# Kernel tuning notes

Measured on AMD Instinct MI355X. Metric: run time of the kernel, lower is better.

## Reference

```python
import jax, jax.numpy as jnp
import numpy as np

B, T, D, H, BAND = 2, 4096, 512, 8, 16
LN_EPS = 1e-5


def setup_inputs() -> dict:
    key = jax.random.key(0)
    k0, k1, k2 = jax.random.split(key, 3)
    x = jax.random.normal(k0, (B, T, D), jnp.float32)
    # nn.MultiheadAttention params: packed in_proj [3D, D] and out_proj [D, D]
    w_in = jax.random.normal(k1, (3 * D, D), jnp.float32) * 0.02
    b_in = jnp.zeros((3 * D,), jnp.float32)
    w_out = jax.random.normal(k2, (D, D), jnp.float32) * 0.02
    b_out = jnp.zeros((D,), jnp.float32)
    ln_g = jnp.ones((D,), jnp.float32)
    ln_b = jnp.zeros((D,), jnp.float32)
    return dict(x=x, ln_g=ln_g, ln_b=ln_b, w_in=w_in, b_in=b_in,
                w_out=w_out, b_out=b_out)


def reference(x, ln_g, ln_b, w_in, b_in, w_out, b_out):
    Bq, Tq, Dq = x.shape
    dh = Dq // H
    # LayerNorm
    mu = jnp.mean(x, axis=-1, keepdims=True)
    var = jnp.mean(jnp.square(x - mu), axis=-1, keepdims=True)
    h = (x - mu) * jax.lax.rsqrt(var + LN_EPS) * ln_g + ln_b
    # packed QKV projection (torch Linear: y = h @ W^T + b)
    qkv = h @ w_in.T + b_in                      # [B, T, 3D]
    q, k, v = jnp.split(qkv, 3, axis=-1)
    to_heads = lambda a: a.reshape(Bq, Tq, H, dh).transpose(0, 2, 1, 3)  # [B,H,T,dh]
    q, k, v = to_heads(q), to_heads(k), to_heads(v)
    # band-gather: each query t attends to keys in [t-BAND, t+BAND]
    Wn = 2 * BAND + 1
    offs = jnp.arange(-BAND, BAND + 1)
    idx = jnp.arange(Tq)[:, None] + offs[None, :]          # [T, Wn]
    valid = (idx >= 0) & (idx < Tq)                        # [T, Wn]
    idx_c = jnp.clip(idx, 0, Tq - 1)
    k_win = k[:, :, idx_c]                                 # [B,H,T,Wn,dh]
    v_win = v[:, :, idx_c]                                 # [B,H,T,Wn,dh]
    scale = 1.0 / np.sqrt(dh).astype(np.float32)
    scores = jnp.einsum('bhtd,bhtwd->bhtw', q * scale, k_win)
    scores = jnp.where(valid[None, None], scores, -jnp.inf)
    p = jax.nn.softmax(scores, axis=-1)                    # [B,H,T,Wn]
    o = jnp.einsum('bhtw,bhtwd->bhtd', p, v_win)           # [B,H,T,dh]
    o = o.transpose(0, 2, 1, 3).reshape(Bq, Tq, Dq)
    y = o @ w_out.T + b_out
    return x + y
```

## Files before the change

kernel.cpp:

```cpp
#include <hip/hip_runtime.h>
#include <hip/hip_bf16.h>

#define T_ 4096
#define D_ 512
#define H_ 8
#define BAND 16
#define G1_K 512

typedef float f32x4 __attribute__((ext_vector_type(4)));
typedef __bf16 bf16x8 __attribute__((ext_vector_type(8)));
typedef unsigned short us8 __attribute__((ext_vector_type(8)));
typedef unsigned short us4 __attribute__((ext_vector_type(4)));

__device__ __forceinline__ unsigned short f2b(float f) {
  union { float f; unsigned u; } v; v.f = f;
  unsigned r = v.u + 0x7fffu + ((v.u >> 16) & 1u);
  return (unsigned short)(r >> 16);
}

__device__ __forceinline__ f32x4 mfma16(bf16x8 a, bf16x8 b, f32x4 c) {
  return __builtin_amdgcn_mfma_f32_16x16x32_bf16(a, b, c, 0, 0, 0);
}

#define GLD16(gp, lp) __builtin_amdgcn_global_load_lds( \
    (const __attribute__((address_space(1))) void*)(gp), \
    (__attribute__((address_space(3))) void*)(lp), 16, 0, 0)

__global__ __launch_bounds__(256) void prep_k(const float* __restrict__ x,
                                              const float* __restrict__ g,
                                              const float* __restrict__ bt,
                                              const float* __restrict__ win,
                                              const float* __restrict__ wout,
                                              unsigned short* __restrict__ h,
                                              unsigned short* __restrict__ winb,
                                              unsigned short* __restrict__ woutb) {
  int bx = blockIdx.x;
  if (bx >= 2048) {
    int i = (bx - 2048) * 256 + threadIdx.x;
    const int n1 = 3 * D_ * D_ / 4;
    if (i < n1) {
      float4 v = ((const float4*)win)[i];
      us4 o; o.x = f2b(v.x); o.y = f2b(v.y); o.z = f2b(v.z); o.w = f2b(v.w);
      ((us4*)winb)[i] = o;
    } else {
      int j = i - n1;
      float4 v = ((const float4*)wout)[j];
      us4 o; o.x = f2b(v.x); o.y = f2b(v.y); o.z = f2b(v.z); o.w = f2b(v.w);
      ((us4*)woutb)[j] = o;
    }
    return;
  }
  int wave = threadIdx.x >> 6, lane = threadIdx.x & 63;
  size_t row = (size_t)bx * 4 + wave;
  const float4* xr = (const float4*)(x + row * D_);
  float4 a = xr[lane * 2], b = xr[lane * 2 + 1];
  float s = a.x + a.y + a.z + a.w + b.x + b.y + b.z + b.w;
  #pragma unroll
  for (int o = 32; o; o >>= 1) s += __shfl_xor(s, o, 64);
  float mu = s * (1.0f / D_);
  float d0 = a.x - mu, d1 = a.y - mu, d2 = a.z - mu, d3 = a.w - mu;
  float d4 = b.x - mu, d5 = b.y - mu, d6 = b.z - mu, d7 = b.w - mu;
  float q = d0*d0 + d1*d1 + d2*d2 + d3*d3 + d4*d4 + d5*d5 + d6*d6 + d7*d7;
  #pragma unroll
  for (int o = 32; o; o >>= 1) q += __shfl_xor(q, o, 64);
  float rstd = rsqrtf(q * (1.0f / D_) + 1e-5f);
  const float4* gr = (const float4*)g;
  const float4* br = (const float4*)bt;
  float4 g0 = gr[lane * 2], g1 = gr[lane * 2 + 1];
  float4 b0 = br[lane * 2], b1 = br[lane * 2 + 1];
  us8 o8;
  o8[0] = f2b(d0 * rstd * g0.x + b0.x);
  o8[1] = f2b(d1 * rstd * g0.y + b0.y);
  o8[2] = f2b(d2 * rstd * g0.z + b0.z);
  o8[3] = f2b(d3 * rstd * g0.w + b0.w);
  o8[4] = f2b(d4 * rstd * g1.x + b1.x);
  o8[5] = f2b(d5 * rstd * g1.y + b1.y);
  o8[6] = f2b(d6 * rstd * g1.z + b1.z);
  o8[7] = f2b(d7 * rstd * g1.w + b1.w);
  *((us8*)(h + row * D_) + lane) = o8;
}

#define OPA 0
#define OPB 1

__device__ __forceinline__ void stg(const unsigned short* __restrict__ gb,
                                    unsigned short* lds, int slot, int op, int h, int tt,
                                    int rl0, int u0, int su) {
  #pragma unroll
  for (int j = 0; j < 2; ++j) {
    const unsigned short* g = gb + (size_t)(h * 128 + rl0 + 64 * j) * G1_K + tt * 64 + su;
    unsigned short* lp = lds + slot * 32768 + op * 16384 + h * 8192 + (rl0 + 64 * j) * 64 + u0 * 8;
    GLD16(g, lp);
  }
}

#define VMC4 asm volatile("s_waitcnt vmcnt(4)" ::: "memory")
#define VMC0 asm volatile("s_waitcnt vmcnt(0)" ::: "memory")

#define PHASE(SLOT, PH, STAGE_STMT, WAIT_STMT) do {                                        \
    if ((PH) == 0) {                                                                       \
      _Pragma("unroll") for (int nf = 0; nf < 4; ++nf) {                                   \
        breg[nf][0] = *(const bf16x8*)(lds + (SLOT)*32768 + boff + nf*1024 + swz0);        \
        breg[nf][1] = *(const bf16x8*)(lds + (SLOT)*32768 + boff + nf*1024 + swz1);        \
      }                                                                                    \
    }                                                                                      \
    bf16x8 a0k0 = *(const bf16x8*)(lds + (SLOT)*32768 + aoff + (2*(PH))*1024 + swz0);      \
    bf16x8 a0k1 = *(const bf16x8*)(lds + (SLOT)*32768 + aoff + (2*(PH))*1024 + swz1);      \
    bf16x8 a1k0 = *(const bf16x8*)(lds + (SLOT)*32768 + aoff + (2*(PH)+1)*1024 + swz0);    \
    bf16x8 a1k1 = *(const bf16x8*)(lds + (SLOT)*32768 + aoff + (2*(PH)+1)*1024 + swz1);    \
    STAGE_STMT;                                                                            \
    __builtin_amdgcn_s_barrier();                                                          \
    asm volatile("s_waitcnt lgkmcnt(0)" ::: "memory");                                     \
    __builtin_amdgcn_sched_barrier(0);                                                     \
    __builtin_amdgcn_s_setprio(1);                                                         \
    _Pragma("unroll") for (int nf = 0; nf < 4; ++nf) {                                     \
      acc[2*(PH)][nf]   = mfma16(a0k0, breg[nf][0], acc[2*(PH)][nf]);                      \
      acc[2*(PH)][nf]   = mfma16(a0k1, breg[nf][1], acc[2*(PH)][nf]);                      \
      acc[2*(PH)+1][nf] = mfma16(a1k0, breg[nf][0], acc[2*(PH)+1][nf]);                    \
      acc[2*(PH)+1][nf] = mfma16(a1k1, breg[nf][1], acc[2*(PH)+1][nf]);                    \
    }                                                                                      \
    __builtin_amdgcn_s_setprio(0);                                                         \
    __builtin_amdgcn_sched_barrier(0);                                                     \
    WAIT_STMT;                                                                             \
    __builtin_amdgcn_s_barrier();                                                          \
  } while (0)

__global__ __launch_bounds__(512, 2) void gemm_qkv8(const unsigned short* __restrict__ A,
                                                    const unsigned short* __restrict__ Bw,
                                                    const float* __restrict__ bias,
                                                    unsigned short* __restrict__ C) {
  extern __shared__ char smem[];
  unsigned short* lds = (unsigned short*)smem;
  int tid = threadIdx.x;
  int lane = tid & 63, wave = tid >> 6;
  int wm = wave >> 2, wn = wave & 3;
  int fr = lane & 15, fq = lane >> 4;
  int d = blockIdx.x;
  int l = (d & 7) * 24 + (d >> 3);
  int bm = l / 6, bn = l % 6;

  const unsigned short* Ag = A + (size_t)bm * 256 * G1_K;
  const unsigned short* Bg = Bw + (size_t)bn * 256 * G1_K;

  int rl0 = tid >> 3, u0 = tid & 7;
  int su = (u0 ^ (rl0 & 7)) * 8;

  int aoff = wm * 8192 + fr * 64;
  int boff = 16384 + (wn >> 1) * 8192 + ((wn & 1) * 64 + fr) * 64;
  int swz0 = (fq ^ (fr & 7)) * 8;
  int swz1 = ((4 + fq) ^ (fr & 7)) * 8;

  f32x4 acc[8][4] = {};
  bf16x8 breg[4][2];

  stg(Bg, lds, 0, OPB, 0, 0, rl0, u0, su);
  stg(Bg, lds, 0, OPB, 1, 0, rl0, u0, su);
  stg(Ag, lds, 0, OPA, 0, 0, rl0, u0, su);
  stg(Ag, lds, 0, OPA, 1, 0, rl0, u0, su);
  stg(Bg, lds, 1, OPB, 0, 1, rl0, u0, su);
  stg(Bg, lds, 1, OPB, 1, 1, rl0, u0, su);
  VMC4;
  __builtin_amdgcn_s_barrier();

  #pragma unroll 1
  for (int i = 0; i < 3; ++i) {
    int t = 2 * i;
    PHASE(0, 0, stg(Ag, lds, 1, OPA, 0, t + 1, rl0, u0, su), (void)0);
    PHASE(0, 1, stg(Ag, lds, 1, OPA, 1, t + 1, rl0, u0, su), (void)0);
    PHASE(0, 2, stg(Bg, lds, 0, OPB, 0, t + 2, rl0, u0, su), (void)0);
    PHASE(0, 3, stg(Bg, lds, 0, OPB, 1, t + 2, rl0, u0, su), VMC4);
    PHASE(1, 0, stg(Ag, lds, 0, OPA, 0, t + 2, rl0, u0, su), (void)0);
    PHASE(1, 1, stg(Ag, lds, 0, OPA, 1, t + 2, rl0, u0, su), (void)0);
    PHASE(1, 2, stg(Bg, lds, 1, OPB, 0, t + 3, rl0, u0, su), (void)0);
    PHASE(1, 3, stg(Bg, lds, 1, OPB, 1, t + 3, rl0, u0, su), VMC4);
  }
  PHASE(0, 0, stg(Ag, lds, 1, OPA, 0, 7, rl0, u0, su), (void)0);
  PHASE(0, 1, stg(Ag, lds, 1, OPA, 1, 7, rl0, u0, su), (void)0);
  PHASE(0, 2, (void)0, (void)0);
  PHASE(0, 3, (void)0, VMC0);
  PHASE(1, 0, (void)0, (void)0);
  PHASE(1, 1, (void)0, (void)0);
  PHASE(1, 2, (void)0, (void)0);
  PHASE(1, 3, (void)0, (void)0);

  int rbase = bm * 256 + wm * 128 + fq * 4;
  int cbase = bn * 256 + wn * 64 + fr;
  float bv[4];
  #pragma unroll
  for (int nf = 0; nf < 4; ++nf) bv[nf] = bias[cbase + nf * 16];
  #pragma unroll
  for (int mf = 0; mf < 8; ++mf)
    #pragma unroll
    for (int nf = 0; nf < 4; ++nf)
      #pragma unroll
      for (int r = 0; r < 4; ++r)
        C[(size_t)(rbase + mf * 16 + r) * 1536 + cbase + nf * 16] = f2b(acc[mf][nf][r] + bv[nf]);
}

__global__ __launch_bounds__(512, 2) void attn_out_k(const unsigned short* __restrict__ qkv,
                                                     const unsigned short* __restrict__ woutb,
                                                     const float* __restrict__ bout,
                                                     const float* __restrict__ x,
                                                     float* __restrict__ out) {
  extern __shared__ char smem2[];
  unsigned short* lds = (unsigned short*)smem2;
  int tid = threadIdx.x;
  int lane = tid & 63, wave = tid >> 6;
  int fr = lane & 15, fq = lane >> 4;
  int r0g = blockIdx.x * 32;
  int bb = r0g >> 12;
  int t0 = r0g & (T_ - 1);
  size_t rowbase = (size_t)bb * T_;

  unsigned short* Ob = lds + 41984;

  #pragma unroll 1
  for (int rd = 0; rd < 2; ++rd) {
    #pragma unroll
    for (int i = 0; i < 8; ++i) {
      int idx = i * 512 + tid;
      int s   = idx >> 10;
      int rem = idx & 1023;
      int ten = rem >> 9;
      int c   = rem & 511;
      int r   = c >> 3, u = c & 7;
      int hh  = 4 * rd + s;
      int tg  = t0 - BAND + r;
      us8 v8 = {0, 0, 0, 0, 0, 0, 0, 0};
      if (tg >= 0 && tg < T_)
        v8 = *(const us8*)(qkv + (rowbase + tg) * 1536 + (ten ? 1024 : 512) + hh * 64 + u * 8);
      if (ten == 0) {
        *(us8*)(lds + s * 8192 + r * 64 + ((u ^ (r & 7)) << 3)) = v8;
      } else {
        int base = s * 8192 + 4096;
        #pragma unroll
        for (int j = 0; j < 8; ++j)
          lds[base + (u * 8 + j) * 64 + (((r >> 3) ^ u) << 3) + (r & 7)] = v8[j];
      }
    }
    __syncthreads();

    {
      int s  = wave >> 1;
      int hh = 4 * rd + s;
      int qg = wave & 1;
      int q  = t0 + qg * 16 + fr;

      const unsigned short* qp = qkv + (rowbase + q) * 1536 + hh * 64;
      bf16x8 qf0 = *(const bf16x8*)(qp + fq * 8);
      bf16x8 qf1 = *(const bf16x8*)(qp + 32 + fq * 8);

      const unsigned short* Kb = lds + s * 8192;
      f32x4 sacc[4];
      #pragma unroll
      for (int mf = 0; mf < 4; ++mf) sacc[mf] = (f32x4){0.f, 0.f, 0.f, 0.f};
      #pragma unroll
      for (int mf = 0; mf < 4; ++mf) {
        bf16x8 k0 = *(const bf16x8*)(Kb + (mf * 16 + fr) * 64 + ((fq ^ (fr & 7)) << 3));
        bf16x8 k1 = *(const bf16x8*)(Kb + (mf * 16 + fr) * 64 + (((4 + fq) ^ (fr & 7)) << 3));
        sacc[mf] = mfma16(k0, qf0, sacc[mf]);
        sacc[mf] = mfma16(k1, qf1, sacc[mf]);
      }

      float ev[4][4];
      float vmx = -1e30f;
      #pragma unroll
      for (int mf = 0; mf < 4; ++mf)
        #pragma unroll
        for (int r = 0; r < 4; ++r) {
          int tk = t0 - BAND + mf * 16 + fq * 4 + r;
          bool ok = (tk >= q - BAND) && (tk <= q + BAND) && (tk >= 0) && (tk < T_);
          float v = ok ? sacc[mf][r] * 0.125f : -1e30f;
          ev[mf][r] = v;
          vmx = fmaxf(vmx, v);
        }
      vmx = fmaxf(vmx, __shfl_xor(vmx, 16, 64));
      vmx = fmaxf(vmx, __shfl_xor(vmx, 32, 64));
      float ssum = 0.f;
      #pragma unroll
      for (int mf = 0; mf < 4; ++mf)
        #pragma unroll
        for (int r = 0; r < 4; ++r) {
          float e = (ev[mf][r] > -1e29f) ? exp2f((ev[mf][r] - vmx) * 1.44269504f) : 0.f;
          ev[mf][r] = e;
          ssum += e;
        }
      ssum += __shfl_xor(ssum, 16, 64);
      ssum += __shfl_xor(ssum, 32, 64);
      float inv = 1.0f / ssum;

      unsigned short* Pb = lds + 32768 + wave * 1152;
      #pragma unroll
      for (int mf = 0; mf < 4; ++mf)
        #pragma unroll
        for (int r = 0; r < 4; ++r)
          Pb[fr * 72 + mf * 16 + fq * 4 + r] = f2b(ev[mf][r] * inv);
      asm volatile("s_waitcnt lgkmcnt(0)" ::: "memory");
      __builtin_amdgcn_sched_barrier(0);

      const unsigned short* Vb = lds + s * 8192 + 4096;
      f32x4 oacc[4];
      #pragma unroll
      for (int cf = 0; cf < 4; ++cf) oacc[cf] = (f32x4){0.f, 0.f, 0.f, 0.f};
      #pragma unroll
      for (int kk = 0; kk < 2; ++kk) {
        bf16x8 pa = *(const bf16x8*)(Pb + fr * 72 + (kk * 4 + fq) * 8);
        #pragma unroll
        for (int cf = 0; cf < 4; ++cf) {
          int du = cf * 2 + (fr >> 3);
          bf16x8 vf = *(const bf16x8*)(Vb + (cf * 16 + fr) * 64 + (((kk * 4 + fq) ^ du) << 3));
          oacc[cf] = mfma16(pa, vf, oacc[cf]);
        }
      }

      #pragma unroll
      for (int cf = 0; cf < 4; ++cf)
        #pragma unroll
        for (int r = 0; r < 4; ++r) {
          int qq = qg * 16 + fq * 4 + r;
          int unit = hh * 8 + (((cf * 2 + (fr >> 3)) ^ (qq & 7)));
          Ob[qq * 512 + unit * 8 + (fr & 7)] = f2b(oacc[cf][r]);
        }
    }
    __syncthreads();
  }

  f32x4 acc[2][4];
  #pragma unroll
  for (int mf = 0; mf < 2; ++mf)
    #pragma unroll
    for (int nf = 0; nf < 4; ++nf) acc[mf][nf] = (f32x4){0.f, 0.f, 0.f, 0.f};

  const unsigned short* Bb = woutb + (size_t)(wave * 64) * 512;
  #pragma unroll 4
  for (int ks = 0; ks < 16; ++ks) {
    bf16x8 a0 = *(const bf16x8*)(Ob + (0 * 16 + fr) * 512 + (((ks * 4 + fq) ^ (fr & 7)) << 3));
    bf16x8 a1 = *(const bf16x8*)(Ob + (1 * 16 + fr) * 512 + (((ks * 4 + fq) ^ (fr & 7)) << 3));
    bf16x8 bfr[4];
    #pragma unroll
    for (int nf = 0; nf < 4; ++nf)
      bfr[nf] = *(const bf16x8*)(Bb + (size_t)(nf * 16 + fr) * 512 + ks * 32 + fq * 8);
    #pragma unroll
    for (int nf = 0; nf < 4; ++nf) {
      acc[0][nf] = mfma16(a0, bfr[nf], acc[0][nf]);
      acc[1][nf] = mfma16(a1, bfr[nf], acc[1][nf]);
    }
  }

  #pragma unroll
  for (int mf = 0; mf < 2; ++mf)
    #pragma unroll
    for (int nf = 0; nf < 4; ++nf) {
      int col = wave * 64 + nf * 16 + fr;
      float bv = bout[col];
      #pragma unroll
      for (int r = 0; r < 4; ++r) {
        size_t e = (size_t)(r0g + mf * 16 + fq * 4 + r) * 512 + col;
        out[e] = x[e] + acc[mf][nf][r] + bv;
      }
    }
}

extern "C" void kernel_launch(void* const* d_in, const int* in_sizes, int n_in,
                              void* d_out, int out_size, void* d_ws, size_t ws_size,
                              hipStream_t stream) {
  (void)in_sizes; (void)n_in; (void)out_size; (void)ws_size;
  const float* x     = (const float*)d_in[0];
  const float* ln_g  = (const float*)d_in[1];
  const float* ln_b  = (const float*)d_in[2];
  const float* w_in  = (const float*)d_in[3];
  const float* b_in  = (const float*)d_in[4];
  const float* w_out = (const float*)d_in[5];
  const float* b_out = (const float*)d_in[6];
  float* out = (float*)d_out;

  char* ws = (char*)d_ws;
  unsigned short* hb    = (unsigned short*)(ws);
  unsigned short* winb  = (unsigned short*)(ws + 8388608);
  unsigned short* woutb = (unsigned short*)(ws + 9961472);
  unsigned short* qkvb  = (unsigned short*)(ws + 10485760);

  (void)hipFuncSetAttribute((const void*)gemm_qkv8,
                            hipFuncAttributeMaxDynamicSharedMemorySize, 131072);
  (void)hipFuncSetAttribute((const void*)attn_out_k,
                            hipFuncAttributeMaxDynamicSharedMemorySize, 116736);

  prep_k<<<3072, 256, 0, stream>>>(x, ln_g, ln_b, w_in, w_out, hb, winb, woutb);
  gemm_qkv8<<<192, 512, 131072, stream>>>(hb, winb, b_in, qkvb);
  attn_out_k<<<256, 512, 116736, stream>>>(qkvb, woutb, b_out, x, out);
}
```

Baseline: 61.77 us.

## Shrink attention blocks to 16 rows, pass P via shuffles, remap block order

The attention+out-projection kernel now processes 16 query rows per block with 256 threads (one wave per head) instead of 32 rows with 512 threads. The key window drops to 48 rows (3 MFMA tiles), so less K/V is staged into LDS. The probability matrix moves from the LDS round-trip to lane shuffles. Block indices are permuted across the grid, and the LDS footprint drops so more blocks fit per CU. The trade-off is that each block redoes the halo K/V loads for fewer queries and re-reads the full W_out for only 16 rows, doubling W_out traffic.

```diff
diff --git a/kernel.cpp b/kernel.cpp
--- a/kernel.cpp
+++ b/kernel.cpp
@@ -197,7 +197,7 @@
         C[(size_t)(rbase + mf * 16 + r) * 1536 + cbase + nf * 16] = f2b(acc[mf][nf][r] + bv[nf]);
 }
 
-__global__ __launch_bounds__(512, 2) void attn_out_k(const unsigned short* __restrict__ qkv,
+__global__ __launch_bounds__(256, 2) void attn_out_k(const unsigned short* __restrict__ qkv,
                                                      const unsigned short* __restrict__ woutb,
                                                      const float* __restrict__ bout,
                                                      const float* __restrict__ x,
@@ -207,32 +207,40 @@
   int tid = threadIdx.x;
   int lane = tid & 63, wave = tid >> 6;
   int fr = lane & 15, fq = lane >> 4;
-  int r0g = blockIdx.x * 32;
+  int dd = blockIdx.x;
+  int lblk = (dd & 7) * 64 + (dd >> 3);
+  int r0g = lblk * 16;
   int bb = r0g >> 12;
   int t0 = r0g & (T_ - 1);
   size_t rowbase = (size_t)bb * T_;
 
-  unsigned short* Ob = lds + 41984;
+  unsigned short* Ob = lds + 28672;
 
   #pragma unroll 1
   for (int rd = 0; rd < 2; ++rd) {
+    if (rd) __syncthreads();
     #pragma unroll
-    for (int i = 0; i < 8; ++i) {
-      int idx = i * 512 + tid;
-      int s   = idx >> 10;
-      int rem = idx & 1023;
-      int ten = rem >> 9;
-      int c   = rem & 511;
-      int r   = c >> 3, u = c & 7;
-      int hh  = 4 * rd + s;
-      int tg  = t0 - BAND + r;
-      us8 v8 = {0, 0, 0, 0, 0, 0, 0, 0};
-      if (tg >= 0 && tg < T_)
-        v8 = *(const us8*)(qkv + (rowbase + tg) * 1536 + (ten ? 1024 : 512) + hh * 64 + u * 8);
-      if (ten == 0) {
-        *(us8*)(lds + s * 8192 + r * 64 + ((u ^ (r & 7)) << 3)) = v8;
+    for (int it = 0; it < 14; ++it) {
+      int idx = it * 256 + tid;
+      if (idx < 1536) {
+        int s = idx / 384, rem = idx % 384;
+        int r = rem >> 3, u = rem & 7;
+        int tg = t0 - BAND + r;
+        int hh = rd * 4 + s;
+        us8 v8 = {0,0,0,0,0,0,0,0};
+        if (tg >= 0 && tg < T_)
+          v8 = *(const us8*)(qkv + (rowbase + tg) * 1536 + 512 + hh * 64 + u * 8);
+        *(us8*)(lds + s * 3072 + r * 64 + ((u ^ (r & 7)) << 3)) = v8;
       } else {
-        int base = s * 8192 + 4096;
+        int i2 = idx - 1536;
+        int s = i2 >> 9, rem = i2 & 511;
+        int r = rem >> 3, u = rem & 7;
+        int tg = t0 - BAND + r;
+        int hh = rd * 4 + s;
+        us8 v8 = {0,0,0,0,0,0,0,0};
+        if (r < 48 && tg >= 0 && tg < T_)
+          v8 = *(const us8*)(qkv + (rowbase + tg) * 1536 + 1024 + hh * 64 + u * 8);
+        int base = 12288 + s * 4096;
         #pragma unroll
         for (int j = 0; j < 8; ++j)
           lds[base + (u * 8 + j) * 64 + (((r >> 3) ^ u) << 3) + (r & 7)] = v8[j];
@@ -241,31 +249,29 @@
     __syncthreads();
 
     {
-      int s  = wave >> 1;
-      int hh = 4 * rd + s;
-      int qg = wave & 1;
-      int q  = t0 + qg * 16 + fr;
+      int hh = rd * 4 + wave;
+      int q  = t0 + fr;
 
       const unsigned short* qp = qkv + (rowbase + q) * 1536 + hh * 64;
       bf16x8 qf0 = *(const bf16x8*)(qp + fq * 8);
       bf16x8 qf1 = *(const bf16x8*)(qp + 32 + fq * 8);
 
-      const unsigned short* Kb = lds + s * 8192;
-      f32x4 sacc[4];
-      #pragma unroll
-      for (int mf = 0; mf < 4; ++mf) sacc[mf] = (f32x4){0.f, 0.f, 0.f, 0.f};
-      #pragma unroll
-      for (int mf = 0; mf < 4; ++mf) {
+      const unsigned short* Kb = lds + wave * 3072;
+      f32x4 sacc[3];
+      #pragma unroll
+      for (int mf = 0; mf < 3; ++mf) sacc[mf] = (f32x4){0.f, 0.f, 0.f, 0.f};
+      #pragma unroll
+      for (int mf = 0; mf < 3; ++mf) {
         bf16x8 k0 = *(const bf16x8*)(Kb + (mf * 16 + fr) * 64 + ((fq ^ (fr & 7)) << 3));
         bf16x8 k1 = *(const bf16x8*)(Kb + (mf * 16 + fr) * 64 + (((4 + fq) ^ (fr & 7)) << 3));
         sacc[mf] = mfma16(k0, qf0, sacc[mf]);
         sacc[mf] = mfma16(k1, qf1, sacc[mf]);
       }
 
-      float ev[4][4];
+      float ev[3][4];
       float vmx = -1e30f;
       #pragma unroll
-      for (int mf = 0; mf < 4; ++mf)
+      for (int mf = 0; mf < 3; ++mf)
         #pragma unroll
         for (int r = 0; r < 4; ++r) {
           int tk = t0 - BAND + mf * 16 + fq * 4 + r;
@@ -278,7 +284,7 @@
       vmx = fmaxf(vmx, __shfl_xor(vmx, 32, 64));
       float ssum = 0.f;
       #pragma unroll
-      for (int mf = 0; mf < 4; ++mf)
+      for (int mf = 0; mf < 3; ++mf)
         #pragma unroll
         for (int r = 0; r < 4; ++r) {
           float e = (ev[mf][r] > -1e29f) ? exp2f((ev[mf][r] - vmx) * 1.44269504f) : 0.f;
@@ -289,76 +295,91 @@
       ssum += __shfl_xor(ssum, 32, 64);
       float inv = 1.0f / ssum;
 
-      unsigned short* Pb = lds + 32768 + wave * 1152;
-      #pragma unroll
-      for (int mf = 0; mf < 4; ++mf)
-        #pragma unroll
-        for (int r = 0; r < 4; ++r)
-          Pb[fr * 72 + mf * 16 + fq * 4 + r] = f2b(ev[mf][r] * inv);
-      asm volatile("s_waitcnt lgkmcnt(0)" ::: "memory");
-      __builtin_amdgcn_sched_barrier(0);
-
-      const unsigned short* Vb = lds + s * 8192 + 4096;
+      int lo[3], hi[3];
+      #pragma unroll
+      for (int mf = 0; mf < 3; ++mf) {
+        lo[mf] = (int)((unsigned)f2b(ev[mf][0] * inv) | ((unsigned)f2b(ev[mf][1] * inv) << 16));
+        hi[mf] = (int)((unsigned)f2b(ev[mf][2] * inv) | ((unsigned)f2b(ev[mf][3] * inv) << 16));
+      }
+
+      int s0 = (((2 * fq) & 3) << 4) | fr;
+      int s1 = (((2 * fq + 1) & 3) << 4) | fr;
+      bool sel0 = (fq < 2);
+      const unsigned short* Vb = lds + 12288 + wave * 4096;
       f32x4 oacc[4];
       #pragma unroll
       for (int cf = 0; cf < 4; ++cf) oacc[cf] = (f32x4){0.f, 0.f, 0.f, 0.f};
-      #pragma unroll
-      for (int kk = 0; kk < 2; ++kk) {
-        bf16x8 pa = *(const bf16x8*)(Pb + fr * 72 + (kk * 4 + fq) * 8);
+
+      union { int w[4]; bf16x8 v; } pa;
+      {
+        int a0 = __shfl(lo[0], s0, 64), a1 = __shfl(lo[1], s0, 64);
+        int b0 = __shfl(hi[0], s0, 64), b1 = __shfl(hi[1], s0, 64);
+        int c0 = __shfl(lo[0], s1, 64), c1 = __shfl(lo[1], s1, 64);
+        int d0 = __shfl(hi[0], s1, 64), d1 = __shfl(hi[1], s1, 64);
+        pa.w[0] = sel0 ? a0 : a1;
+        pa.w[1] = sel0 ? b0 : b1;
+        pa.w[2] = sel0 ? c0 : c1;
+        pa.w[3] = sel0 ? d0 : d1;
         #pragma unroll
         for (int cf = 0; cf < 4; ++cf) {
-          int du = cf * 2 + (fr >> 3);
-          bf16x8 vf = *(const bf16x8*)(Vb + (cf * 16 + fr) * 64 + (((kk * 4 + fq) ^ du) << 3));
-          oacc[cf] = mfma16(pa, vf, oacc[cf]);
+          int dcol = cf * 16 + fr;
+          bf16x8 vf = *(const bf16x8*)(Vb + dcol * 64 + ((fq ^ (dcol >> 3)) << 3));
+          oacc[cf] = mfma16(pa.v, vf, oacc[cf]);
         }
       }
+      {
+        int a2 = __shfl(lo[2], s0, 64), b2 = __shfl(hi[2], s0, 64);
+        int c2 = __shfl(lo[2], s1, 64), d2 = __shfl(hi[2], s1, 64);
+        pa.w[0] = sel0 ? a2 : 0;
+        pa.w[1] = sel0 ? b2 : 0;
+        pa.w[2] = sel0 ? c2 : 0;
+        pa.w[3] = sel0 ? d2 : 0;
+        #pragma unroll
+        for (int cf = 0; cf < 4; ++cf) {
+          int dcol = cf * 16 + fr;
+          bf16x8 vf = *(const bf16x8*)(Vb + dcol * 64 + (((4 + fq) ^ (dcol >> 3)) << 3));
+          oacc[cf] = mfma16(pa.v, vf, oacc[cf]);
+        }
+      }
 
       #pragma unroll
       for (int cf = 0; cf < 4; ++cf)
         #pragma unroll
         for (int r = 0; r < 4; ++r) {
-          int qq = qg * 16 + fq * 4 + r;
-          int unit = hh * 8 + (((cf * 2 + (fr >> 3)) ^ (qq & 7)));
-          Ob[qq * 512 + unit * 8 + (fr & 7)] = f2b(oacc[cf][r]);
+          int ql = fq * 4 + r;
+          int gl = cf * 2 + (fr >> 3);
+          Ob[ql * 512 + (hh * 8 + (gl ^ (ql & 7))) * 8 + (fr & 7)] = f2b(oacc[cf][r]);
         }
     }
-    __syncthreads();
-  }
-
-  f32x4 acc[2][4];
-  #pragma unroll
-  for (int mf = 0; mf < 2; ++mf)
-    #pragma unroll
-    for (int nf = 0; nf < 4; ++nf) acc[mf][nf] = (f32x4){0.f, 0.f, 0.f, 0.f};
-
-  const unsigned short* Bb = woutb + (size_t)(wave * 64) * 512;
+  }
+  __syncthreads();
+
+  f32x4 acc[8];
+  #pragma unroll
+  for (int nf = 0; nf < 8; ++nf) acc[nf] = (f32x4){0.f, 0.f, 0.f, 0.f};
+  const unsigned short* Bb = woutb + (size_t)(wave * 128) * 512;
   #pragma unroll 4
   for (int ks = 0; ks < 16; ++ks) {
-    bf16x8 a0 = *(const bf16x8*)(Ob + (0 * 16 + fr) * 512 + (((ks * 4 + fq) ^ (fr & 7)) << 3));
-    bf16x8 a1 = *(const bf16x8*)(Ob + (1 * 16 + fr) * 512 + (((ks * 4 + fq) ^ (fr & 7)) << 3));
-    bf16x8 bfr[4];
+    bf16x8 a0 = *(const bf16x8*)(Ob + fr * 512 + (((ks * 4 + fq) ^ (fr & 7)) << 3));
+    bf16x8 bfr[8];
     #pragma unroll
-    for (int nf = 0; nf < 4; ++nf)
+    for (int nf = 0; nf < 8; ++nf)
       bfr[nf] = *(const bf16x8*)(Bb + (size_t)(nf * 16 + fr) * 512 + ks * 32 + fq * 8);
     #pragma unroll
-    for (int nf = 0; nf < 4; ++nf) {
-      acc[0][nf] = mfma16(a0, bfr[nf], acc[0][nf]);
-      acc[1][nf] = mfma16(a1, bfr[nf], acc[1][nf]);
+    for (int nf = 0; nf < 8; ++nf)
+      acc[nf] = mfma16(a0, bfr[nf], acc[nf]);
+  }
+
+  #pragma unroll
+  for (int nf = 0; nf < 8; ++nf) {
+    int col = wave * 128 + nf * 16 + fr;
+    float bv = bout[col];
+    #pragma unroll
+    for (int r = 0; r < 4; ++r) {
+      size_t e = (size_t)(r0g + fq * 4 + r) * 512 + col;
+      out[e] = x[e] + acc[nf][r] + bv;
     }
   }
-
-  #pragma unroll
-  for (int mf = 0; mf < 2; ++mf)
-    #pragma unroll
-    for (int nf = 0; nf < 4; ++nf) {
-      int col = wave * 64 + nf * 16 + fr;
-      float bv = bout[col];
-      #pragma unroll
-      for (int r = 0; r < 4; ++r) {
-        size_t e = (size_t)(r0g + mf * 16 + fq * 4 + r) * 512 + col;
-        out[e] = x[e] + acc[mf][nf][r] + bv;
-      }
-    }
 }
 
 extern "C" void kernel_launch(void* const* d_in, const int* in_sizes, int n_in,
@@ -383,9 +404,9 @@
   (void)hipFuncSetAttribute((const void*)gemm_qkv8,
                             hipFuncAttributeMaxDynamicSharedMemorySize, 131072);
   (void)hipFuncSetAttribute((const void*)attn_out_k,
-                            hipFuncAttributeMaxDynamicSharedMemorySize, 116736);
+                            hipFuncAttributeMaxDynamicSharedMemorySize, 73728);
 
   prep_k<<<3072, 256, 0, stream>>>(x, ln_g, ln_b, w_in, w_out, hb, winb, woutb);
   gemm_qkv8<<<192, 512, 131072, stream>>>(hb, winb, b_in, qkvb);
-  attn_out_k<<<256, 512, 116736, stream>>>(qkvb, woutb, b_out, x, out);
-}
+  attn_out_k<<<512, 256, 73728, stream>>>(qkvb, woutb, b_out, x, out);
+}
```

After: 75.80 us. 22.7% more time.
